# Performance work log

Measured on AMD Instinct MI355X. Metric: run time of the kernel, lower is better.

The kernel has to match this reference:

```python
import jax, jax.numpy as jnp
import numpy as np

B, D, H, Z, E = 65536, 128, 256, 128, 16  # batch, input, hidden, hyper, embedding


def setup_inputs() -> dict:
    key = jax.random.key(0)
    ks = jax.random.split(key, 20)
    s = 0.02  # small weight scale for numerical sanity
    return {
        "x": jax.random.normal(ks[0], (B, D), jnp.float32),
        "h0": jax.random.normal(ks[1], (B, H), jnp.float32),
        "c0": jax.random.normal(ks[2], (B, H), jnp.float32),
        "hhat0": jax.random.normal(ks[3], (B, Z), jnp.float32),
        "chat0": jax.random.normal(ks[4], (B, Z), jnp.float32),
        "hweight": jax.random.normal(ks[5], (Z + H + D, 4 * Z), jnp.float32) * s,
        "hbias": jnp.zeros((4 * Z,), jnp.float32),
        "zw_h": jax.random.normal(ks[6], (Z, 4 * E), jnp.float32) * s,
        "zw_x": jax.random.normal(ks[7], (Z, 4 * E), jnp.float32) * s,
        "zw_b": jax.random.normal(ks[8], (Z, 4 * E), jnp.float32) * 0.01,
        "zb_h": jnp.ones((4 * E,), jnp.float32),
        "zb_x": jnp.ones((4 * E,), jnp.float32),
        "dw_h": jnp.full((4, E, H), 0.1 / E, jnp.float32),  # [i,g,f,o] stacked
        "dw_x": jnp.full((4, E, H), 0.1 / E, jnp.float32),
        "dw_b": jax.random.normal(ks[9], (4, E, H), jnp.float32) * s,
        "weight": jax.random.normal(ks[10], (H + D, 4 * H), jnp.float32) * s,
        "bias": jnp.zeros((4 * H,), jnp.float32),
    }


def reference(x, h0, c0, hhat0, chat0, hweight, hbias, zw_h, zw_x, zw_b,
              zb_h, zb_x, dw_h, dw_x, dw_b, weight, bias):
    sig, tanh = jax.nn.sigmoid, jnp.tanh
    b = x.shape[0]
    # hyper LSTM cell
    gh = jnp.concatenate([hhat0, h0, x], axis=1) @ hweight + hbias  # [B, 4Z]
    i_h, g_h, f_h, o_h = jnp.split(gh, 4, axis=1)
    chat1 = sig(f_h) * chat0 + sig(i_h) * tanh(g_h)
    hhat1 = sig(o_h) * tanh(chat1)
    # embedding projections z (chunk order i,g,f,o -> reshape to [B,4,E])
    z_h = (hhat1 @ zw_h + zb_h).reshape(b, 4, E)
    z_x = (hhat1 @ zw_x + zb_x).reshape(b, 4, E)
    z_b = (hhat1 @ zw_b).reshape(b, 4, E)
    # d scaling vectors, [B,4,H] -> [B,4H]
    d_yh = jnp.einsum('bke,keh->bkh', z_h, dw_h).reshape(b, 4 * H)
    d_yx = jnp.einsum('bke,keh->bkh', z_x, dw_x).reshape(b, 4 * H)
    d_yb = jnp.einsum('bke,keh->bkh', z_b, dw_b).reshape(b, 4 * H)
    # main LSTM gates, hyper-modulated
    g = jnp.concatenate([h0, x], axis=1) @ weight * d_yh * d_yx + d_yb + bias
    i_g, g_g, f_g, o_g = jnp.split(g, 4, axis=1)
    c1 = sig(f_g) * c0 + sig(i_g) * tanh(g_g)
    h1 = sig(o_g) * tanh(c1)
    return (h1, c1, hhat1, chat1)
```

## Files before the change

kernel.cpp:

```cpp
#include <hip/hip_runtime.h>


typedef unsigned short u16;
typedef __attribute__((ext_vector_type(8))) short bf16x8;
typedef __attribute__((ext_vector_type(4))) float f32x4;

#define BATCH 65536

__device__ __forceinline__ u16 f2b(float f) {
  unsigned u = __float_as_uint(f);
  u += 0x7fffu + ((u >> 16) & 1u);
  return (u16)(u >> 16);
}
__device__ __forceinline__ unsigned pk2(float a, float b) {
  return (unsigned)f2b(a) | ((unsigned)f2b(b) << 16);
}
__device__ __forceinline__ float upk_lo(unsigned u) { return __uint_as_float(u << 16); }
__device__ __forceinline__ float upk_hi(unsigned u) { return __uint_as_float(u & 0xffff0000u); }
__device__ __forceinline__ float sigf(float x) { return 1.0f / (1.0f + __expf(-x)); }
__device__ __forceinline__ float tanhfast(float x) {
  float xc = fminf(fmaxf(x, -15.f), 15.f);
  float e = __expf(2.f * xc);
  return (e - 1.f) / (e + 1.f);
}
__device__ __forceinline__ int swz(int r, int c) { return r * 64 + (c ^ ((r & 7) << 3)); }

#define VM_BAR(N) do { \
  asm volatile("s_waitcnt vmcnt(" #N ")" ::: "memory"); \
  __builtin_amdgcn_s_barrier(); \
  __builtin_amdgcn_sched_barrier(0); } while (0)

__device__ __forceinline__ void gl_lds16(const u16* g, u16* l) {
  __builtin_amdgcn_global_load_lds(
      (const __attribute__((address_space(1))) void*)g,
      (__attribute__((address_space(3))) void*)l, 16, 0, 0);
}
__device__ __forceinline__ void stageA(const u16* base, int ldk, u16* lA, int t) {
  const int r = t >> 3, q = t & 7, wid = t >> 6;
  const int qs = (q ^ (r & 7)) << 3;
  gl_lds16(base + (size_t)r * ldk + qs, lA + wid * 512);
  gl_lds16(base + (size_t)(r + 32) * ldk + qs, lA + 2048 + wid * 512);
}

__global__ __launch_bounds__(256) void hlstm_pre(
    const float* __restrict__ hhat0, const float* __restrict__ h0,
    const float* __restrict__ x, u16* __restrict__ abuf,
    const float* __restrict__ hweight, const float* __restrict__ hbias,
    const float* __restrict__ zw_h, const float* __restrict__ zw_x, const float* __restrict__ zw_b,
    const float* __restrict__ zb_h, const float* __restrict__ zb_x,
    const float* __restrict__ dw_h, const float* __restrict__ dw_x, const float* __restrict__ dw_b,
    const float* __restrict__ weight, const float* __restrict__ bias,
    u16* __restrict__ hw_fr, float* __restrict__ hbias_r,
    u16* __restrict__ w_fr,  float* __restrict__ bias_r,
    u16* __restrict__ whp_fr, u16* __restrict__ wxp_fr, u16* __restrict__ wbp_fr,
    float* __restrict__ bhp_r, float* __restrict__ bxp_r)
{
  if (blockIdx.x < 4096) {
    const size_t stride = (size_t)4096 * 256;
    for (size_t i = (size_t)blockIdx.x * 256 + threadIdx.x;
         i < (size_t)BATCH * 64; i += stride) {
      const size_t b = i >> 6; const int c = (int)(i & 63);
      const float* src;
      if (c < 16)      src = hhat0 + b * 128 + c * 8;
      else if (c < 48) src = h0 + b * 256 + (size_t)(c - 16) * 8;
      else             src = x + b * 128 + (size_t)(c - 48) * 8;
      float4 v0 = ((const float4*)src)[0];
      float4 v1 = ((const float4*)src)[1];
      alignas(16) u16 o[8] = {f2b(v0.x), f2b(v0.y), f2b(v0.z), f2b(v0.w),
                              f2b(v1.x), f2b(v1.y), f2b(v1.z), f2b(v1.w)};
      *(uint4*)(abuf + i * 8) = *(const uint4*)o;
    }
    return;
  }
  const int tid = (blockIdx.x - 4096) * 256 + threadIdx.x;
  const int nt  = 512 * 256;

  for (int i = tid; i < 16 * 16384; i += nt) {
    int tile = i >> 14, r = i & 16383;
    int wc = r >> 12, h = (r >> 11) & 1, g = (r >> 9) & 3;
    int lane = (r >> 3) & 63, j = r & 7;
    int hb = tile >> 3, s = tile & 7;
    int k = s * 64 + h * 32 + (lane >> 4) * 8 + j;
    int col = g * 128 + hb * 64 + wc * 16 + (lane & 15);
    hw_fr[i] = f2b(hweight[k * 512 + col]);
  }
  for (int i = tid; i < 24 * 16384; i += nt) {
    int tile = i >> 14, r = i & 16383;
    int wc = r >> 12, h = (r >> 11) & 1, g = (r >> 9) & 3;
    int lane = (r >> 3) & 63, j = r & 7;
    int hb = tile / 6, s = tile % 6;
    int k = s * 64 + h * 32 + (lane >> 4) * 8 + j;
    int col = g * 256 + hb * 64 + wc * 16 + (lane & 15);
    w_fr[i] = f2b(weight[k * 1024 + col]);
  }
  for (int i = tid; i < 3 * 8 * 16384; i += nt) {
    int mat = i / (8 * 16384), rem = i % (8 * 16384);
    int tile = rem >> 14, r = rem & 16383;
    int wc = r >> 12, h = (r >> 11) & 1, g = (r >> 9) & 3;
    int lane = (r >> 3) & 63, j = r & 7;
    int hb = tile >> 1, s = tile & 1;
    int k = s * 64 + h * 32 + (lane >> 4) * 8 + j;
    int colh = hb * 64 + wc * 16 + (lane & 15);
    const float* zw = (mat == 0) ? zw_h : (mat == 1) ? zw_x : zw_b;
    const float* dw = (mat == 0) ? dw_h : (mat == 1) ? dw_x : dw_b;
    float sv = 0.f;
#pragma unroll
    for (int e = 0; e < 16; ++e)
      sv += zw[k * 64 + g * 16 + e] * dw[g * 4096 + e * 256 + colh];
    u16* dst = (mat == 0) ? whp_fr : (mat == 1) ? wxp_fr : wbp_fr;
    dst[rem] = f2b(sv);
  }
  for (int i = tid; i < 1024; i += nt) {
    int hb = i >> 8, g = (i >> 6) & 3, hh = i & 63;
    int h = hb * 64 + hh;
    float sh = 0.f, sx = 0.f;
#pragma unroll
    for (int e = 0; e < 16; ++e) {
      sh += zb_h[g * 16 + e] * dw_h[g * 4096 + e * 256 + h];
      sx += zb_x[g * 16 + e] * dw_x[g * 4096 + e * 256 + h];
    }
    bhp_r[i] = sh; bxp_r[i] = sx;
    bias_r[i] = bias[g * 256 + h];
  }
  for (int i = tid; i < 512; i += nt) {
    int gate = (i >> 6) & 3, hb = i >> 8, hh = i & 63;
    hbias_r[i] = hbias[gate * 128 + hb * 64 + hh];
  }
}

__global__ __launch_bounds__(256, 3) void hlstm_k1(
    const u16* __restrict__ abuf, const float* __restrict__ chat0,
    const u16* __restrict__ hw_fr, const float* __restrict__ hbias_r,
    float* __restrict__ d_out, u16* __restrict__ hbuf)
{
  __shared__ alignas(16) u16 lA[3][64 * 64];
  const int f = blockIdx.x;
  const int xcd = f & 7, s2 = f >> 3;
  const int rb = xcd * 128 + (s2 >> 1), hb = s2 & 1;
  const int t = threadIdx.x;
  const int lane = t & 63, wc = t >> 6;
  const int lr = lane & 15, kg = lane >> 4;

  f32x4 acc[4][4];
  const f32x4 zzero = {0.f, 0.f, 0.f, 0.f};
#pragma unroll
  for (int mf = 0; mf < 4; ++mf)
#pragma unroll
    for (int g = 0; g < 4; ++g) acc[mf][g] = zzero;

  const u16* arow = abuf + (size_t)rb * 64 * 512;

  bf16x8 breg[8];
  auto loadB = [&](const u16* bt) {
#pragma unroll
    for (int h = 0; h < 2; ++h)
#pragma unroll
      for (int g = 0; g < 4; ++g)
        breg[h * 4 + g] = *(const bf16x8*)&bt[((wc * 2 + h) * 4 + g) * 512 + lane * 8];
  };
  auto sweep = [&](f32x4 (&ac)[4][4], const u16* cA) {
    __builtin_amdgcn_s_setprio(1);
#pragma unroll
    for (int h = 0; h < 2; ++h)
#pragma unroll
      for (int mf = 0; mf < 4; ++mf) {
        bf16x8 afr = *(const bf16x8*)&cA[swz(mf * 16 + lr, h * 32 + kg * 8)];
#pragma unroll
        for (int g = 0; g < 4; ++g)
          ac[mf][g] = __builtin_amdgcn_mfma_f32_16x16x32_bf16(afr, breg[h * 4 + g], ac[mf][g], 0, 0, 0);
      }
    __builtin_amdgcn_s_setprio(0);
  };

  stageA(arow + 0 * 64, 512, lA[0], t);
  stageA(arow + 1 * 64, 512, lA[1], t);
  loadB(hw_fr + (size_t)(hb * 8 + 0) * 16384);
  VM_BAR(8);

#pragma unroll
  for (int ks = 0; ks < 8; ++ks) {
    if (ks < 6) stageA(arow + (ks + 2) * 64, 512, lA[(ks + 2) % 3], t);
    sweep(acc, lA[ks % 3]);
    if (ks < 7) loadB(hw_fr + (size_t)(hb * 8 + ks + 1) * 16384);
    if (ks < 6)       VM_BAR(10);
    else if (ks == 6) VM_BAR(8);
  }

  float hb4[4];
#pragma unroll
  for (int g = 0; g < 4; ++g) hb4[g] = hbias_r[hb * 256 + g * 64 + wc * 16 + lr];
  const int zc = hb * 64 + wc * 16 + lr;
  float* out_hh = d_out + (size_t)BATCH * 512;
  float* out_ch = d_out + (size_t)BATCH * 640;
#pragma unroll
  for (int mf = 0; mf < 4; ++mf)
#pragma unroll
    for (int r = 0; r < 4; ++r) {
      const int row = rb * 64 + mf * 16 + kg * 4 + r;
      const float gi = acc[mf][0][r] + hb4[0];
      const float gg = acc[mf][1][r] + hb4[1];
      const float gf = acc[mf][2][r] + hb4[2];
      const float go = acc[mf][3][r] + hb4[3];
      const float c0v = chat0[(size_t)row * 128 + zc];
      const float c1v = sigf(gf) * c0v + sigf(gi) * tanhfast(gg);
      const float h1v = sigf(go) * tanhfast(c1v);
      out_hh[(size_t)row * 128 + zc] = h1v;
      out_ch[(size_t)row * 128 + zc] = c1v;
      hbuf[(size_t)row * 128 + zc] = f2b(h1v);
    }
}

__global__ __launch_bounds__(256, 3) void hlstm_k2(
    const u16* __restrict__ abuf, const u16* __restrict__ hbuf,
    const float* __restrict__ c0,
    const u16* __restrict__ w_fr, const float* __restrict__ bias_r,
    const u16* __restrict__ whp_fr, const u16* __restrict__ wxp_fr, const u16* __restrict__ wbp_fr,
    const float* __restrict__ bhp_r, const float* __restrict__ bxp_r,
    float* __restrict__ d_out)
{
  __shared__ alignas(16) u16 lA[2][64 * 64];
  __shared__ alignas(16) unsigned ldsc[8192];
  const int f = blockIdx.x;
  const int xcd = f & 7, s4 = f >> 3;
  const int rb = xcd * 128 + (s4 >> 2), hb = s4 & 3;
  const int t = threadIdx.x;
  const int lane = t & 63, wc = t >> 6;
  const int lr = lane & 15, kg = lane >> 4;

  const u16* amain = abuf + (size_t)rb * 64 * 512 + 128;
  const u16* ahyp  = hbuf + (size_t)rb * 64 * 128;

  auto aptr = [&](int s) -> const u16* {
    if (s >= 4 && s < 10) return amain + (s - 4) * 64;
    return ahyp + (s & 1) * 64;
  };
  auto aldk = [&](int s) -> int { return (s >= 4 && s < 10) ? 512 : 128; };
  auto bptr = [&](int s) -> const u16* {
    if (s < 2)  return whp_fr + (size_t)(hb * 2 + s) * 16384;
    if (s < 4)  return wxp_fr + (size_t)(hb * 2 + s - 2) * 16384;
    if (s < 10) return w_fr  + (size_t)(hb * 6 + s - 4) * 16384;
    return wbp_fr + (size_t)(hb * 2 + s - 10) * 16384;
  };

  f32x4 acc[4][4];
  const f32x4 zzero = {0.f, 0.f, 0.f, 0.f};
#pragma unroll
  for (int mf = 0; mf < 4; ++mf)
#pragma unroll
    for (int g = 0; g < 4; ++g) acc[mf][g] = zzero;

  bf16x8 breg[8];
  auto loadB = [&](const u16* bt) {
#pragma unroll
    for (int h = 0; h < 2; ++h)
#pragma unroll
      for (int g = 0; g < 4; ++g)
        breg[h * 4 + g] = *(const bf16x8*)&bt[((wc * 2 + h) * 4 + g) * 512 + lane * 8];
  };
  auto sweep = [&](f32x4 (&ac)[4][4], const u16* cA) {
    __builtin_amdgcn_s_setprio(1);
#pragma unroll
    for (int h = 0; h < 2; ++h)
#pragma unroll
      for (int mf = 0; mf < 4; ++mf) {
        bf16x8 afr = *(const bf16x8*)&cA[swz(mf * 16 + lr, h * 32 + kg * 8)];
#pragma unroll
        for (int g = 0; g < 4; ++g)
          ac[mf][g] = __builtin_amdgcn_mfma_f32_16x16x32_bf16(afr, breg[h * 4 + g], ac[mf][g], 0, 0, 0);
      }
    __builtin_amdgcn_s_setprio(0);
  };

  stageA(aptr(0), aldk(0), lA[0], t);
  loadB(bptr(0));
  VM_BAR(8);

#pragma unroll
  for (int s = 0; s < 12; ++s) {
    if (s < 11) stageA(aptr(s + 1), aldk(s + 1), lA[(s + 1) & 1], t);
    if (s == 2 || s == 4) {
#pragma unroll
      for (int mf = 0; mf < 4; ++mf)
#pragma unroll
        for (int g = 0; g < 4; ++g) acc[mf][g] = zzero;
    }
    sweep(acc, lA[s & 1]);
    if (s < 11) loadB(bptr(s + 1));

    if (s == 1) {
      float bh4[4];
#pragma unroll
      for (int g = 0; g < 4; ++g) bh4[g] = bhp_r[hb * 256 + g * 64 + wc * 16 + lr];
#pragma unroll
      for (int mf = 0; mf < 4; ++mf)
#pragma unroll
        for (int gp = 0; gp < 2; ++gp) {
          const int g0 = gp * 2, g1 = gp * 2 + 1;
          uint4 v;
          v.x = pk2(acc[mf][g0][0] + bh4[g0], acc[mf][g0][1] + bh4[g0]);
          v.y = pk2(acc[mf][g0][2] + bh4[g0], acc[mf][g0][3] + bh4[g0]);
          v.z = pk2(acc[mf][g1][0] + bh4[g1], acc[mf][g1][1] + bh4[g1]);
          v.w = pk2(acc[mf][g1][2] + bh4[g1], acc[mf][g1][3] + bh4[g1]);
          *(uint4*)&ldsc[(mf * 2 + gp) * 1024 + t * 4] = v;
        }
    } else if (s == 3) {
      float bx4[4];
#pragma unroll
      for (int g = 0; g < 4; ++g) bx4[g] = bxp_r[hb * 256 + g * 64 + wc * 16 + lr];
#pragma unroll
      for (int mf = 0; mf < 4; ++mf)
#pragma unroll
        for (int gp = 0; gp < 2; ++gp) {
          const int g0 = gp * 2, g1 = gp * 2 + 1;
          uint4 v = *(const uint4*)&ldsc[(mf * 2 + gp) * 1024 + t * 4];
          v.x = pk2(upk_lo(v.x) * (acc[mf][g0][0] + bx4[g0]),
                    upk_hi(v.x) * (acc[mf][g0][1] + bx4[g0]));
          v.y = pk2(upk_lo(v.y) * (acc[mf][g0][2] + bx4[g0]),
                    upk_hi(v.y) * (acc[mf][g0][3] + bx4[g0]));
          v.z = pk2(upk_lo(v.z) * (acc[mf][g1][0] + bx4[g1]),
                    upk_hi(v.z) * (acc[mf][g1][1] + bx4[g1]));
          v.w = pk2(upk_lo(v.w) * (acc[mf][g1][2] + bx4[g1]),
                    upk_hi(v.w) * (acc[mf][g1][3] + bx4[g1]));
          *(uint4*)&ldsc[(mf * 2 + gp) * 1024 + t * 4] = v;
        }
    } else if (s == 9) {
#pragma unroll
      for (int mf = 0; mf < 4; ++mf)
#pragma unroll
        for (int gp = 0; gp < 2; ++gp) {
          const int g0 = gp * 2, g1 = gp * 2 + 1;
          uint4 v = *(const uint4*)&ldsc[(mf * 2 + gp) * 1024 + t * 4];
          acc[mf][g0][0] *= upk_lo(v.x);
          acc[mf][g0][1] *= upk_hi(v.x);
          acc[mf][g0][2] *= upk_lo(v.y);
          acc[mf][g0][3] *= upk_hi(v.y);
          acc[mf][g1][0] *= upk_lo(v.z);
          acc[mf][g1][1] *= upk_hi(v.z);
          acc[mf][g1][2] *= upk_lo(v.w);
          acc[mf][g1][3] *= upk_hi(v.w);
        }
    }
    if (s < 11) VM_BAR(8);
  }

  const int hcol = hb * 64 + wc * 16 + lr;
  float b4[4];
#pragma unroll
  for (int g = 0; g < 4; ++g) b4[g] = bias_r[hb * 256 + g * 64 + wc * 16 + lr];
  float* out_c1 = d_out + (size_t)BATCH * 256;
#pragma unroll
  for (int mf = 0; mf < 4; ++mf)
#pragma unroll
    for (int r = 0; r < 4; ++r) {
      const int row = rb * 64 + mf * 16 + kg * 4 + r;
      const float gi = acc[mf][0][r] + b4[0];
      const float gg = acc[mf][1][r] + b4[1];
      const float gf = acc[mf][2][r] + b4[2];
      const float go = acc[mf][3][r] + b4[3];
      const float c0v = c0[(size_t)row * 256 + hcol];
      const float c1v = sigf(gf) * c0v + sigf(gi) * tanhfast(gg);
      const float h1v = sigf(go) * tanhfast(c1v);
      d_out[(size_t)row * 256 + hcol]  = h1v;
      out_c1[(size_t)row * 256 + hcol] = c1v;
    }
}

extern "C" void kernel_launch(void* const* d_in, const int* in_sizes, int n_in,
                              void* d_out, int out_size, void* d_ws, size_t ws_size,
                              hipStream_t stream)
{
  (void)in_sizes; (void)n_in; (void)out_size; (void)ws_size;
  const float* x       = (const float*)d_in[0];
  const float* h0      = (const float*)d_in[1];
  const float* c0      = (const float*)d_in[2];
  const float* hhat0   = (const float*)d_in[3];
  const float* chat0   = (const float*)d_in[4];
  const float* hweight = (const float*)d_in[5];
  const float* hbias   = (const float*)d_in[6];
  const float* zw_h    = (const float*)d_in[7];
  const float* zw_x    = (const float*)d_in[8];
  const float* zw_b    = (const float*)d_in[9];
  const float* zb_h    = (const float*)d_in[10];
  const float* zb_x    = (const float*)d_in[11];
  const float* dw_h    = (const float*)d_in[12];
  const float* dw_x    = (const float*)d_in[13];
  const float* dw_b    = (const float*)d_in[14];
  const float* weight  = (const float*)d_in[15];
  const float* bias    = (const float*)d_in[16];

  char* wsb = (char*)d_ws;
  u16*   abuf    = (u16*)(wsb + 0);
  u16*   hbuf    = (u16*)(wsb + 67108864);
  u16*   hw_fr   = (u16*)(wsb + 83886080);
  u16*   w_fr    = (u16*)(wsb + 84410368);
  u16*   whp_fr  = (u16*)(wsb + 85196800);
  u16*   wxp_fr  = (u16*)(wsb + 85458944);
  u16*   wbp_fr  = (u16*)(wsb + 85721088);
  float* hbias_r = (float*)(wsb + 85983232);
  float* bias_r  = (float*)(wsb + 85985280);
  float* bhp_r   = (float*)(wsb + 85989376);
  float* bxp_r   = (float*)(wsb + 85993472);

  hlstm_pre<<<dim3(4608), dim3(256), 0, stream>>>(
      hhat0, h0, x, abuf,
      hweight, hbias, zw_h, zw_x, zw_b, zb_h, zb_x, dw_h, dw_x, dw_b, weight, bias,
      hw_fr, hbias_r, w_fr, bias_r, whp_fr, wxp_fr, wbp_fr, bhp_r, bxp_r);

  hlstm_k1<<<dim3(2048), dim3(256), 0, stream>>>(
      abuf, chat0, hw_fr, hbias_r, (float*)d_out, hbuf);

  hlstm_k2<<<dim3(4096), dim3(256), 0, stream>>>(
      abuf, hbuf, c0, w_fr, bias_r, whp_fr, wxp_fr, wbp_fr, bhp_r, bxp_r, (float*)d_out);
}
```

Before: 264.2 us.

## Split B-fragment loads per half-K, prefetch cell state, reuse staged hyper tiles

Both GEMM kernels now hold the B fragments in two half-K register sets. The next step's half is loaded right after the matching MFMA half-sweep, so global loads overlap the remaining MFMAs. The chat0/c0 values for the epilogue are loaded into registers before the last sweep instead of inside the epilogue. In the main LSTM kernel, steps 2 and 3 reread the same hhat1 chunks already sitting in the two LDS buffers, so their A staging is dropped. The split loads lean on the vmcnt barrier counts staying correct, and the prefetched state adds register pressure under the 3-wave occupancy bound.

```diff
diff --git a/kernel.cpp b/kernel.cpp
--- a/kernel.cpp
+++ b/kernel.cpp
@@ -150,46 +150,53 @@
 
   const u16* arow = abuf + (size_t)rb * 64 * 512;
 
-  bf16x8 breg[8];
-  auto loadB = [&](const u16* bt) {
-#pragma unroll
-    for (int h = 0; h < 2; ++h)
+  bf16x8 B0[4], B1[4];
+  f32x4 chr[4];
+  auto loadBh = [&](bf16x8 (&Bh)[4], const u16* bt, int h) {
+#pragma unroll
+    for (int g = 0; g < 4; ++g)
+      Bh[g] = *(const bf16x8*)&bt[((wc * 2 + h) * 4 + g) * 512 + lane * 8];
+  };
+  auto sweepH = [&](int h, const bf16x8 (&Bh)[4], const u16* cA) {
+#pragma unroll
+    for (int mf = 0; mf < 4; ++mf) {
+      bf16x8 afr = *(const bf16x8*)&cA[swz(mf * 16 + lr, h * 32 + kg * 8)];
 #pragma unroll
       for (int g = 0; g < 4; ++g)
-        breg[h * 4 + g] = *(const bf16x8*)&bt[((wc * 2 + h) * 4 + g) * 512 + lane * 8];
-  };
-  auto sweep = [&](f32x4 (&ac)[4][4], const u16* cA) {
-    __builtin_amdgcn_s_setprio(1);
-#pragma unroll
-    for (int h = 0; h < 2; ++h)
-#pragma unroll
-      for (int mf = 0; mf < 4; ++mf) {
-        bf16x8 afr = *(const bf16x8*)&cA[swz(mf * 16 + lr, h * 32 + kg * 8)];
-#pragma unroll
-        for (int g = 0; g < 4; ++g)
-          ac[mf][g] = __builtin_amdgcn_mfma_f32_16x16x32_bf16(afr, breg[h * 4 + g], ac[mf][g], 0, 0, 0);
-      }
-    __builtin_amdgcn_s_setprio(0);
-  };
+        acc[mf][g] = __builtin_amdgcn_mfma_f32_16x16x32_bf16(afr, Bh[g], acc[mf][g], 0, 0, 0);
+    }
+  };
+
+  const int zc = hb * 64 + wc * 16 + lr;
 
   stageA(arow + 0 * 64, 512, lA[0], t);
   stageA(arow + 1 * 64, 512, lA[1], t);
-  loadB(hw_fr + (size_t)(hb * 8 + 0) * 16384);
-  VM_BAR(8);
+  loadBh(B0, hw_fr + (size_t)(hb * 8 + 0) * 16384, 0);
+  loadBh(B1, hw_fr + (size_t)(hb * 8 + 0) * 16384, 1);
+  VM_BAR(10);
 
 #pragma unroll
   for (int ks = 0; ks < 8; ++ks) {
     if (ks < 6) stageA(arow + (ks + 2) * 64, 512, lA[(ks + 2) % 3], t);
-    sweep(acc, lA[ks % 3]);
-    if (ks < 7) loadB(hw_fr + (size_t)(hb * 8 + ks + 1) * 16384);
-    if (ks < 6)       VM_BAR(10);
-    else if (ks == 6) VM_BAR(8);
+    if (ks == 7) {
+#pragma unroll
+      for (int mf = 0; mf < 4; ++mf)
+#pragma unroll
+        for (int r = 0; r < 4; ++r)
+          chr[mf][r] = chat0[(size_t)(rb * 64 + mf * 16 + kg * 4 + r) * 128 + zc];
+    }
+    __builtin_amdgcn_s_setprio(1);
+    sweepH(0, B0, lA[ks % 3]);
+    if (ks < 7) loadBh(B0, hw_fr + (size_t)(hb * 8 + ks + 1) * 16384, 0);
+    sweepH(1, B1, lA[ks % 3]);
+    if (ks < 7) loadBh(B1, hw_fr + (size_t)(hb * 8 + ks + 1) * 16384, 1);
+    __builtin_amdgcn_s_setprio(0);
+    if (ks < 7) VM_BAR(10);
   }
 
   float hb4[4];
 #pragma unroll
   for (int g = 0; g < 4; ++g) hb4[g] = hbias_r[hb * 256 + g * 64 + wc * 16 + lr];
-  const int zc = hb * 64 + wc * 16 + lr;
   float* out_hh = d_out + (size_t)BATCH * 512;
   float* out_ch = d_out + (size_t)BATCH * 640;
 #pragma unroll
@@ -201,8 +208,7 @@
       const float gg = acc[mf][1][r] + hb4[1];
       const float gf = acc[mf][2][r] + hb4[2];
       const float go = acc[mf][3][r] + hb4[3];
-      const float c0v = chat0[(size_t)row * 128 + zc];
-      const float c1v = sigf(gf) * c0v + sigf(gi) * tanhfast(gg);
+      const float c1v = sigf(gf) * chr[mf][r] + sigf(gi) * tanhfast(gg);
       const float h1v = sigf(go) * tanhfast(c1v);
       out_hh[(size_t)row * 128 + zc] = h1v;
       out_ch[(size_t)row * 128 + zc] = c1v;
@@ -249,43 +255,53 @@
 #pragma unroll
     for (int g = 0; g < 4; ++g) acc[mf][g] = zzero;
 
-  bf16x8 breg[8];
-  auto loadB = [&](const u16* bt) {
-#pragma unroll
-    for (int h = 0; h < 2; ++h)
+  bf16x8 B0[4], B1[4];
+  f32x4 c0r[4];
+  auto loadBh = [&](bf16x8 (&Bh)[4], const u16* bt, int h) {
+#pragma unroll
+    for (int g = 0; g < 4; ++g)
+      Bh[g] = *(const bf16x8*)&bt[((wc * 2 + h) * 4 + g) * 512 + lane * 8];
+  };
+  auto sweepH = [&](int h, const bf16x8 (&Bh)[4], const u16* cA) {
+#pragma unroll
+    for (int mf = 0; mf < 4; ++mf) {
+      bf16x8 afr = *(const bf16x8*)&cA[swz(mf * 16 + lr, h * 32 + kg * 8)];
 #pragma unroll
       for (int g = 0; g < 4; ++g)
-        breg[h * 4 + g] = *(const bf16x8*)&bt[((wc * 2 + h) * 4 + g) * 512 + lane * 8];
-  };
-  auto sweep = [&](f32x4 (&ac)[4][4], const u16* cA) {
+        acc[mf][g] = __builtin_amdgcn_mfma_f32_16x16x32_bf16(afr, Bh[g], acc[mf][g], 0, 0, 0);
+    }
+  };
+
+  const int hcol = hb * 64 + wc * 16 + lr;
+
+  stageA(aptr(0), aldk(0), lA[0], t);
+  stageA(aptr(1), aldk(1), lA[1], t);
+  loadBh(B0, bptr(0), 0);
+  loadBh(B1, bptr(0), 1);
+  VM_BAR(10);
+
+#pragma unroll
+  for (int s = 0; s < 12; ++s) {
+    if (s >= 3 && s < 11) stageA(aptr(s + 1), aldk(s + 1), lA[(s + 1) & 1], t);
+    if (s == 2 || s == 4) {
+#pragma unroll
+      for (int mf = 0; mf < 4; ++mf)
+#pragma unroll
+        for (int g = 0; g < 4; ++g) acc[mf][g] = zzero;
+    }
+    if (s == 11) {
+#pragma unroll
+      for (int mf = 0; mf < 4; ++mf)
+#pragma unroll
+        for (int r = 0; r < 4; ++r)
+          c0r[mf][r] = c0[(size_t)(rb * 64 + mf * 16 + kg * 4 + r) * 256 + hcol];
+    }
     __builtin_amdgcn_s_setprio(1);
-#pragma unroll
-    for (int h = 0; h < 2; ++h)
-#pragma unroll
-      for (int mf = 0; mf < 4; ++mf) {
-        bf16x8 afr = *(const bf16x8*)&cA[swz(mf * 16 + lr, h * 32 + kg * 8)];
-#pragma unroll
-        for (int g = 0; g < 4; ++g)
-          ac[mf][g] = __builtin_amdgcn_mfma_f32_16x16x32_bf16(afr, breg[h * 4 + g], ac[mf][g], 0, 0, 0);
-      }
+    sweepH(0, B0, lA[s & 1]);
+    if (s < 11) loadBh(B0, bptr(s + 1), 0);
+    sweepH(1, B1, lA[s & 1]);
+    if (s < 11) loadBh(B1, bptr(s + 1), 1);
     __builtin_amdgcn_s_setprio(0);
-  };
-
-  stageA(aptr(0), aldk(0), lA[0], t);
-  loadB(bptr(0));
-  VM_BAR(8);
-
-#pragma unroll
-  for (int s = 0; s < 12; ++s) {
-    if (s < 11) stageA(aptr(s + 1), aldk(s + 1), lA[(s + 1) & 1], t);
-    if (s == 2 || s == 4) {
-#pragma unroll
-      for (int mf = 0; mf < 4; ++mf)
-#pragma unroll
-        for (int g = 0; g < 4; ++g) acc[mf][g] = zzero;
-    }
-    sweep(acc, lA[s & 1]);
-    if (s < 11) loadB(bptr(s + 1));
 
     if (s == 1) {
       float bh4[4];
@@ -343,7 +359,6 @@
     if (s < 11) VM_BAR(8);
   }
 
-  const int hcol = hb * 64 + wc * 16 + lr;
   float b4[4];
 #pragma unroll
   for (int g = 0; g < 4; ++g) b4[g] = bias_r[hb * 256 + g * 64 + wc * 16 + lr];
@@ -357,8 +372,7 @@
       const float gg = acc[mf][1][r] + b4[1];
       const float gf = acc[mf][2][r] + b4[2];
       const float go = acc[mf][3][r] + b4[3];
-      const float c0v = c0[(size_t)row * 256 + hcol];
-      const float c1v = sigf(gf) * c0v + sigf(gi) * tanhfast(gg);
+      const float c1v = sigf(gf) * c0r[mf][r] + sigf(gi) * tanhfast(gg);
       const float h1v = sigf(go) * tanhfast(c1v);
       d_out[(size_t)row * 256 + hcol]  = h1v;
       out_c1[(size_t)row * 256 + hcol] = c1v;
```

Result: slower. 328.1 us (+24.2%).
